# Kernel optimization log

Hardware: AMD Instinct MI355X
Metric: run time of the kernel (lower is better)

Reference implementation:

```python
import jax, jax.numpy as jnp
import numpy as np

B, C, H, W = 64, 128, 11, 11
OUT = 16
N_SIM = 5
EPS = 1e-2


def _conv3d(x, w, b):
    # x: [b,ci,D,h,w], w: [co,ci,7,3,3], 'same' padding, ReLU
    y = jax.lax.conv_general_dilated(x, w, (1, 1, 1), [(3, 3), (1, 1), (1, 1)],
                                     dimension_numbers=('NCDHW', 'OIDHW', 'NCDHW'))
    return jax.nn.relu(y + b[None, :, None, None, None])


def _conv2d(x, w, b, dil=1):
    p = dil  # 3x3 kernel, 'same' with dilation
    y = jax.lax.conv_general_dilated(x, w, (1, 1), [(p, p), (p, p)], rhs_dilation=(dil, dil),
                                     dimension_numbers=('NCHW', 'OIHW', 'NCHW'))
    return y + b[None, :, None, None]


def _center(f):  # [b,c,h,w] -> [b,c] (center pixel)
    return f[:, :, f.shape[2] // 2, f.shape[3] // 2]


def _ratio(v):  # compute_ratio_withstep: [b,c] -> [b,1,c,c] band-ratio image
    d = v[:, None, :]
    d = jnp.where(jnp.abs(d) < EPS, EPS, d)
    return (v[:, :, None] / d)[:, None, :, :]


def _cpr(sa3d, w):  # CVT3D_2D_SA: spectral-attention collapse [b,16,D,h,w] -> [b,16,h,w]
    a = jax.nn.softmax(w, axis=-1)
    return jax.nn.relu(jnp.einsum('bodhw,od->bohw', sa3d, a))


def _sideout(f2d, w, b):  # sideout2d: mlp on center pixel features
    return _center(f2d) @ w.T + b


def _similar_sum(x, feat, n=N_SIM):
    # topk(n, largest=False) over |feat - center|, gather those pixels from x, sum them
    b, c = x.shape[0], x.shape[1]
    cv = _center(feat).reshape(b, 1, 1, 1)
    diff = jnp.abs(feat - cv).reshape(b, -1)          # [b, h*w]
    _, idx = jax.lax.top_k(-diff, n)                   # n smallest -> [b, n]
    img = x.reshape(b, c, -1)                          # [b, c, h*w]
    idx_b = jnp.broadcast_to(idx[:, None, :], (b, c, n))
    sim = jnp.take_along_axis(img, idx_b, axis=2)      # [b, c, n]
    return sim.sum(axis=2)                             # masked sum over n similar pixels


def _forward(x, w3d1, b3d1, w3d23, b3d23, cpr_w, w2d45, b2d45, seg_w, seg_b,
             so_w, so_b, sp_wa, sp_ba, sp_wb, sp_bb, sp_sw, sp_sb, fuse_para):
    sp_ct = _ratio(_center(x))                         # [b,1,c,c]
    sa1 = _conv3d(x[:, None], w3d1, b3d1)              # [b,16,C,11,11]
    sa1_2d = _cpr(sa1, cpr_w[0])
    sa2 = _conv3d(sa1, w3d23[0], b3d23[0])
    sa2_2d = _cpr(sa2, cpr_w[1])
    sa3 = _conv3d(sa2, w3d23[1], b3d23[1])
    sa3_2d = _cpr(sa3, cpr_w[2])
    sa4_2d = jax.nn.relu(_conv2d(sa3_2d, w2d45[0], b2d45[0]))
    sa5_2d = jax.nn.relu(_conv2d(sa4_2d, w2d45[1], b2d45[1]))

    feats = [sa1_2d, sa2_2d, sa3_2d, sa4_2d, sa5_2d]
    sa_sides, sp_sides = [], []
    for i, f in enumerate(feats):  # fixed 5 structurally-distinct stages
        sa_sides.append(_sideout(f, so_w[i], so_b[i]))
        act = _conv2d(f, seg_w[i], seg_b[i])           # Seg_Conv: [b,1,11,11]
        s = _similar_sum(x, act)                       # [b,C]
        img = jnp.concatenate([_ratio(s), sp_ct], 1)   # [b,2,C,C]
        y = jax.nn.relu(_conv2d(img, sp_wa[i], sp_ba[i], dil=1))
        y = jax.nn.relu(_conv2d(y, sp_wb[i], sp_bb[i], dil=2))
        sp_sides.append(_sideout(y, sp_sw[i], sp_sb[i]))

    sides = sa_sides + sp_sides
    total = sides[0] * fuse_para[0]
    for i in range(1, 10):
        total = total + fuse_para[i] * sides[i]
    return total                                       # [b, OUT]


def setup_inputs() -> dict:
    key = jax.random.key(0)
    ks = jax.random.split(key, 20)
    s = 0.05
    return {
        'x': jax.random.normal(ks[0], (B, C, H, W), jnp.float32),
        'w3d1': jax.random.normal(ks[1], (16, 1, 7, 3, 3), jnp.float32) * s,
        'b3d1': jnp.zeros((16,), jnp.float32),
        'w3d23': jax.random.normal(ks[2], (2, 16, 16, 7, 3, 3), jnp.float32) * s,
        'b3d23': jnp.zeros((2, 16), jnp.float32),
        'cpr_w': jax.random.normal(ks[3], (3, 16, C), jnp.float32) * s,
        'w2d45': jax.random.normal(ks[4], (2, 16, 16, 3, 3), jnp.float32) * s,
        'b2d45': jnp.zeros((2, 16), jnp.float32),
        'seg_w': jax.random.normal(ks[5], (5, 1, 16, 3, 3), jnp.float32) * s,
        'seg_b': jnp.zeros((5, 1), jnp.float32),
        'so_w': jax.random.normal(ks[6], (5, OUT, 16), jnp.float32) * s,
        'so_b': jnp.zeros((5, OUT), jnp.float32),
        'sp_wa': jax.random.normal(ks[7], (5, 16, 2, 3, 3), jnp.float32) * s,
        'sp_ba': jnp.zeros((5, 16), jnp.float32),
        'sp_wb': jax.random.normal(ks[8], (5, 16, 16, 3, 3), jnp.float32) * s,
        'sp_bb': jnp.zeros((5, 16), jnp.float32),
        'sp_sw': jax.random.normal(ks[9], (5, OUT, 16), jnp.float32) * s,
        'sp_sb': jnp.zeros((5, OUT), jnp.float32),
        'fuse_para': jnp.ones((15,), jnp.float32),
    }


def reference(x, w3d1, b3d1, w3d23, b3d23, cpr_w, w2d45, b2d45, seg_w, seg_b,
              so_w, so_b, sp_wa, sp_ba, sp_wb, sp_bb, sp_sw, sp_sb, fuse_para):
    return _forward(x, w3d1, b3d1, w3d23, b3d23, cpr_w, w2d45, b2d45, seg_w, seg_b,
                    so_w, so_b, sp_wa, sp_ba, sp_wb, sp_bb, sp_sw, sp_sb, fuse_para)
```

## Files before the change

### kernel.cpp

```cpp
#include <hip/hip_runtime.h>
#include <hip/hip_bf16.h>


#define F_SLICE (64 * 16 * 121)
#define PKE (64 * 121 * 134 * 16)
#define LHALF 18304
#define AREP_CV 36864
#define XPADE (64 * 121 * 136)

typedef _Float16 half8 __attribute__((ext_vector_type(8)));
typedef float float4v __attribute__((ext_vector_type(4)));
typedef unsigned short u16x8 __attribute__((ext_vector_type(8)));
typedef unsigned short u16x4 __attribute__((ext_vector_type(4)));

typedef __attribute__((address_space(1))) unsigned int gu32;
typedef __attribute__((address_space(3))) unsigned int lu32;

union HU { _Float16 h; unsigned short u; };

__global__ __launch_bounds__(256) void prep_kernel(
    const float* __restrict__ x, const float* __restrict__ cpr_w,
    const float* __restrict__ w3d1, const float* __restrict__ w2d45,
    const float* __restrict__ w3d23, float* __restrict__ x_t,
    float* __restrict__ a_sm, float* __restrict__ wrep2d,
    unsigned short* __restrict__ arep, unsigned short* __restrict__ arep1,
    unsigned short* __restrict__ xpadh, unsigned short* __restrict__ xpadl,
    unsigned short* __restrict__ zpage) {
  const int bx = blockIdx.x, t = threadIdx.x;
  if (bx < 64) {
    __shared__ float tile[128][123];
    const int b = bx;
    const float* xb = x + (size_t)b * 128 * 121;
    for (int idx = t; idx < 128 * 121; idx += 256) {
      int c = idx / 121, p = idx - c * 121;
      tile[c][p] = xb[idx];
    }
    __syncthreads();
    float* ob = x_t + (size_t)b * 121 * 128;
    for (int idx = t; idx < 121 * 128; idx += 256) {
      int p = idx >> 7, c = idx & 127;
      ob[idx] = tile[c][p];
    }
    unsigned short* xh = xpadh + (size_t)b * 16456;
    unsigned short* xl = xpadl + (size_t)b * 16456;
    for (int idx = t; idx < 16456; idx += 256) {
      int p = idx / 136, d = idx - p * 136;
      float v = 0.f;
      if (d >= 3 && d < 131) v = tile[d - 3][p] * 256.f;
      _Float16 hi = (_Float16)v;
      HU a2, b2;
      a2.h = hi;
      b2.h = (_Float16)(v - (float)hi);
      xh[idx] = a2.u;
      xl[idx] = b2.u;
    }
  } else if (bx < 112) {
    __shared__ float red[128];
    const int row = bx - 64;
    float v = (t < 128) ? cpr_w[row * 128 + t] : -3.0e38f;
    if (t < 128) red[t] = v;
    __syncthreads();
    for (int s = 64; s; s >>= 1) {
      if (t < s) red[t] = fmaxf(red[t], red[t + s]);
      __syncthreads();
    }
    float m = red[0];
    __syncthreads();
    float e = (t < 128) ? expf(v - m) : 0.f;
    if (t < 128) red[t] = e;
    __syncthreads();
    for (int s = 64; s; s >>= 1) {
      if (t < s) red[t] += red[t + s];
      __syncthreads();
    }
    if (t < 128) a_sm[row * 128 + t] = e / red[0];
  } else if (bx < 142) {
    int r = (bx - 112) * 256 + t;
    if (r < 3072) {
      int j = r & 7;
      int lane = (r >> 3) & 63;
      int part = (r >> 9) & 1;
      int kh = r >> 10;
      int m = lane & 15, q = lane >> 4;
      float w = 0.f;
      if (q < 3 && j < 7) w = w3d1[m * 63 + j * 9 + kh * 3 + q] * 256.f;
      _Float16 hi = (_Float16)w;
      HU o;
      o.h = part ? (_Float16)(w - (float)hi) : hi;
      arep1[r] = o.u;
    } else if (r < 3072 + 4608) {
      int r2 = r - 3072;
      int o = r2 & 15;
      int uv = (r2 >> 4) % 9;
      int ic = (r2 / 144) % 16;
      int layer = r2 / 2304;
      wrep2d[r2] = w2d45[((layer * 16 + o) * 16 + ic) * 9 + uv];
    }
  } else if (bx < 430) {
    int idx = (bx - 142) * 256 + t;
    if (idx < 2 * AREP_CV) {
      int j = idx & 7;
      int lane = (idx >> 3) & 63;
      int part = (idx >> 9) & 1;
      int rem = idx >> 10;
      int chunk = rem % 36;
      int cv = rem / 36;
      int kw = chunk % 3;
      int grp = chunk / 3;
      int kdp = grp & 3;
      int kh = grp >> 2;
      int m = lane & 15, q = lane >> 4;
      int kd = 2 * kdp + (q >> 1);
      int ic = (q & 1) * 8 + j;
      float w = 0.f;
      if (kd < 7)
        w = w3d23[((cv * 16 + m) * 16 + ic) * 63 + kd * 9 + kh * 3 + kw] *
            256.f;
      _Float16 hi = (_Float16)w;
      HU out;
      out.h = (part == 0) ? hi : (_Float16)(w - (float)hi);
      arep[idx] = out.u;
    }
  } else {
    if (t < 128) {
      u16x8 z = {0, 0, 0, 0, 0, 0, 0, 0};
      *(u16x8*)&zpage[t * 8] = z;
    }
  }
}

__global__ __launch_bounds__(512, 2) void conv1_mfma_kernel(
    const unsigned short* __restrict__ xph,
    const unsigned short* __restrict__ xpl,
    const unsigned short* __restrict__ arep1, const float* __restrict__ bias,
    const float* __restrict__ al, unsigned short* __restrict__ pk_hi,
    unsigned short* __restrict__ pk_lo, float* __restrict__ fpart) {
  __shared__ _Float16 lds1[104 * 256];
  const int t = threadIdx.x;
  const int bx = blockIdx.x, gy = blockIdx.y, b = blockIdx.z;
  const int lane = t & 63, wave = t >> 6;
  const int n = lane & 15, q = lane >> 4;
  const int hs = wave >> 2, wg = wave & 3;
  const int h = 2 * bx + hs;
  const int D0 = gy * 32;

  {
    const int g = t & 31;
    const int s = g & 7;
    const int w0 = t >> 5;
#pragma unroll
    for (int k = 0; k < 7; ++k) {
      int wid = w0 + k * 16;
      if (wid < 104) {
        int part = wid >= 52;
        int w2 = wid - part * 52;
        int rr = w2 / 13;
        int cc = w2 - rr * 13;
        int hh = 2 * bx - 1 + rr, ww = cc - 1;
        u16x8 v0 = {0, 0, 0, 0, 0, 0, 0, 0};
        u16x8 v1 = {0, 0, 0, 0, 0, 0, 0, 0};
        if (hh >= 0 && hh < 11 && ww >= 0 && ww < 11) {
          const unsigned short* src = (part ? xpl : xph) +
                                      ((size_t)b * 121 + hh * 11 + ww) * 136 +
                                      D0 + (g & ~7);
          v0 = *(const u16x8*)src;
          v1 = *(const u16x8*)(src + 8);
        }
        u16x8 ov;
#define SHIFT_CASE(S)                                                   \
  case S: {                                                             \
    _Pragma("unroll") for (int e = 0; e < 8; ++e) ov[e] =               \
        (((S) + e) < 8) ? v0[((S) + e) & 7] : v1[((S) + e) & 7];        \
  } break;
        switch (s) {
          SHIFT_CASE(0)
          SHIFT_CASE(1)
          SHIFT_CASE(2)
          SHIFT_CASE(3)
          SHIFT_CASE(4)
          SHIFT_CASE(5)
          SHIFT_CASE(6)
          SHIFT_CASE(7)
        }
#undef SHIFT_CASE
        *(u16x8*)&lds1[wid * 256 + g * 8] = ov;
      }
    }
  }

  half8 ahi[3], alo[3];
#pragma unroll
  for (int kh = 0; kh < 3; ++kh) {
    ahi[kh] = *(const half8*)&arep1[(kh * 2 + 0) * 512 + lane * 8];
    alo[kh] = *(const half8*)&arep1[(kh * 2 + 1) * 512 + lane * 8];
  }
  int colq[3];
#pragma unroll
  for (int tt = 0; tt < 3; ++tt) {
    int c = wg * 3 + tt + q;
    colq[tt] = (c > 12) ? 12 : c;
  }
  float bias_r[4];
#pragma unroll
  for (int r = 0; r < 4; ++r) bias_r[r] = bias[q * 4 + r];
  __syncthreads();

#pragma unroll
  for (int d16loc = 0; d16loc < 2; ++d16loc) {
    const int d16g = gy * 2 + d16loc;
    const int dbase = d16loc * 16 + n;
    float4v acc[3];
#pragma unroll
    for (int tt = 0; tt < 3; ++tt) acc[tt] = (float4v){0.f, 0.f, 0.f, 0.f};
#pragma unroll
    for (int kh = 0; kh < 3; ++kh) {
      const int rowoff = (hs + kh) * 13;
#pragma unroll
      for (int tt = 0; tt < 3; ++tt) {
        const int wid = rowoff + colq[tt];
        half8 bh = *(const half8*)&lds1[wid * 256 + dbase * 8];
        half8 bl = *(const half8*)&lds1[(wid + 52) * 256 + dbase * 8];
        acc[tt] =
            __builtin_amdgcn_mfma_f32_16x16x32_f16(ahi[kh], bh, acc[tt], 0, 0, 0);
        acc[tt] =
            __builtin_amdgcn_mfma_f32_16x16x32_f16(ahi[kh], bl, acc[tt], 0, 0, 0);
        acc[tt] =
            __builtin_amdgcn_mfma_f32_16x16x32_f16(alo[kh], bh, acc[tt], 0, 0, 0);
      }
    }
    float alr[4];
#pragma unroll
    for (int r = 0; r < 4; ++r)
      alr[r] = al[(q * 4 + r) * 128 + d16g * 16 + n];
#pragma unroll
    for (int tt = 0; tt < 3; ++tt) {
      const int wl = wg * 3 + tt;
      if (h < 11 && wl < 11) {
        const int p = h * 11 + wl;
        float fr[4];
        u16x4 hi4, lo4;
#pragma unroll
        for (int r = 0; r < 4; ++r) {
          float sv = fmaxf(acc[tt][r] * (1.f / 65536.f) + bias_r[r], 0.f);
          fr[r] = sv * alr[r];
          float sc = sv * 256.f;
          _Float16 hh = (_Float16)sc;
          HU a2, b2;
          a2.h = hh;
          b2.h = (_Float16)(sc - (float)hh);
          hi4[r] = a2.u;
          lo4[r] = b2.u;
        }
        size_t base =
            (((size_t)b * 121 + p) * 134 + d16g * 16 + n + 3) * 16 + q * 4;
        *(u16x4*)&pk_hi[base] = hi4;
        *(u16x4*)&pk_lo[base] = lo4;
        u16x4 z = {0, 0, 0, 0};
        if (d16g == 0 && n < 3) {
          size_t hb = (((size_t)b * 121 + p) * 134 + n) * 16 + q * 4;
          *(u16x4*)&pk_hi[hb] = z;
          *(u16x4*)&pk_lo[hb] = z;
        }
        if (d16g == 7 && n >= 13) {
          size_t hb = (((size_t)b * 121 + p) * 134 + n + 118) * 16 + q * 4;
          *(u16x4*)&pk_hi[hb] = z;
          *(u16x4*)&pk_lo[hb] = z;
        }
#pragma unroll
        for (int r = 0; r < 4; ++r) {
          float v = fr[r];
          v += __shfl_xor(v, 1, 64);
          v += __shfl_xor(v, 2, 64);
          v += __shfl_xor(v, 4, 64);
          v += __shfl_xor(v, 8, 64);
          if (n == 0)
            fpart[(((size_t)d16g * 64 + b) * 16 + q * 4 + r) * 121 + p] = v;
        }
      }
    }
  }
}

template <bool WRITE_PK>
__global__ __launch_bounds__(512, 2) void conv_mfma_kernel(
    const unsigned short* __restrict__ pin_hi,
    const unsigned short* __restrict__ pin_lo,
    const unsigned short* __restrict__ arep, const float* __restrict__ bias,
    const float* __restrict__ al, const unsigned short* __restrict__ zpage,
    unsigned short* __restrict__ pout_hi, unsigned short* __restrict__ pout_lo,
    float* __restrict__ fpart) {
  __shared__ _Float16 lds[2 * LHALF];
  const int t = threadIdx.x;
  const int bx = blockIdx.x, d16 = blockIdx.y, b = blockIdx.z;
  const int lane = t & 63, wave = t >> 6;
  const int n = lane & 15, q = lane >> 4;
  const int hs = wave >> 2, wg = wave & 3;
  const int h = 2 * bx + hs;

#pragma unroll
  for (int i = 0; i < 9; ++i) {
    int u = t + i * 512;
    int lbo = __builtin_amdgcn_readfirstlane((wave << 6) + i * 512);
    if (u < 4576) {
      int part = (u >= 2288) ? 1 : 0;
      int qq = u - part * 2288;
      int panel = qq / 44;
      int rem = qq - panel * 44;
      int dloc = rem >> 1;
      int icq = rem & 1;
      int rr = panel / 13, cc = panel - rr * 13;
      int hh = 2 * bx + rr - 1, ww = cc - 1;
      bool ok = (hh >= 0) & (hh < 11) & (ww >= 0) & (ww < 11);
      const unsigned short* srcp = part ? pin_lo : pin_hi;
      const unsigned short* g =
          ok ? &srcp[(((size_t)b * 121 + hh * 11 + ww) * 134 + d16 * 16 +
                      dloc) *
                         16 +
                     icq * 8]
             : zpage;
      __builtin_amdgcn_global_load_lds((const gu32*)g,
                                       (lu32*)&lds[(size_t)lbo * 8], 16, 0, 0);
    }
  }
  float bias_r[4], alr[4];
#pragma unroll
  for (int r = 0; r < 4; ++r) {
    bias_r[r] = bias[q * 4 + r];
    alr[r] = al[(q * 4 + r) * 128 + d16 * 16 + n];
  }
  __syncthreads();

  const int wl0 = wg * 3;
  int cb[5], cbk[5];
  const int base_qn = (q & 1) * 8 + n * 16 + hs * 4576;
  const int kdh = (lane & 32) ? 16 : 0;
#pragma unroll
  for (int j = 0; j < 5; ++j) {
    int colj = wl0 + j;
    if (colj > 12) colj = 12;
    cb[j] = base_qn + colj * 352;
    cbk[j] = cb[j] + kdh;
  }

  float4v acc[3];
#pragma unroll
  for (int tt = 0; tt < 3; ++tt) acc[tt] = (float4v){0.f, 0.f, 0.f, 0.f};

#pragma unroll
  for (int kh = 0; kh < 3; ++kh) {
#pragma unroll
    for (int kdp = 0; kdp < 4; ++kdp) {
      half8 whi[5], wlo[5];
#pragma unroll
      for (int j = 0; j < 5; ++j) {
        int a = ((kdp < 3) ? cbk[j] : cb[j]) + kh * 4576 + kdp * 32;
        whi[j] = *(const half8*)&lds[a];
        wlo[j] = *(const half8*)&lds[a + LHALF];
      }
#pragma unroll
      for (int kw = 0; kw < 3; ++kw) {
        const int c2 = (kh * 4 + kdp) * 3 + kw;
        half8 ahi = *(const half8*)&arep[((c2 * 2 + 0) * 64 + lane) * 8];
        half8 alo = *(const half8*)&arep[((c2 * 2 + 1) * 64 + lane) * 8];
#pragma unroll
        for (int tt = 0; tt < 3; ++tt) {
          const int jj = tt + kw;
          acc[tt] = __builtin_amdgcn_mfma_f32_16x16x32_f16(ahi, whi[jj],
                                                           acc[tt], 0, 0, 0);
          acc[tt] = __builtin_amdgcn_mfma_f32_16x16x32_f16(ahi, wlo[jj],
                                                           acc[tt], 0, 0, 0);
          acc[tt] = __builtin_amdgcn_mfma_f32_16x16x32_f16(alo, whi[jj],
                                                           acc[tt], 0, 0, 0);
        }
      }
    }
  }

#pragma unroll
  for (int tt = 0; tt < 3; ++tt) {
    const int wl = wg * 3 + tt;
    if (h < 11 && wl < 11) {
      const int p = h * 11 + wl;
      float fr[4];
      u16x4 hi4, lo4;
#pragma unroll
      for (int r = 0; r < 4; ++r) {
        float sv = fmaxf(acc[tt][r] * (1.f / 65536.f) + bias_r[r], 0.f);
        fr[r] = sv * alr[r];
        if (WRITE_PK) {
          float s = sv * 256.f;
          _Float16 hh = (_Float16)s;
          HU a, bb;
          a.h = hh;
          bb.h = (_Float16)(s - (float)hh);
          hi4[r] = a.u;
          lo4[r] = bb.u;
        }
      }
      if (WRITE_PK) {
        size_t base =
            (((size_t)b * 121 + p) * 134 + d16 * 16 + n + 3) * 16 + q * 4;
        *(u16x4*)&pout_hi[base] = hi4;
        *(u16x4*)&pout_lo[base] = lo4;
        u16x4 z = {0, 0, 0, 0};
        if (d16 == 0 && n < 3) {
          size_t hb = (((size_t)b * 121 + p) * 134 + n) * 16 + q * 4;
          *(u16x4*)&pout_hi[hb] = z;
          *(u16x4*)&pout_lo[hb] = z;
        }
        if (d16 == 7 && n >= 13) {
          size_t hb = (((size_t)b * 121 + p) * 134 + n + 118) * 16 + q * 4;
          *(u16x4*)&pout_hi[hb] = z;
          *(u16x4*)&pout_lo[hb] = z;
        }
      }
#pragma unroll
      for (int r = 0; r < 4; ++r) {
        float v = fr[r];
        v += __shfl_xor(v, 1, 64);
        v += __shfl_xor(v, 2, 64);
        v += __shfl_xor(v, 4, 64);
        v += __shfl_xor(v, 8, 64);
        if (n == 0)
          fpart[(((size_t)d16 * 64 + b) * 16 + q * 4 + r) * 121 + p] = v;
      }
    }
  }
}

__global__ __launch_bounds__(128) void sp_prep_kernel(
    const float* __restrict__ fpart0, const float* __restrict__ fpart1,
    const float* __restrict__ fpart2, const float* __restrict__ x_t,
    const float* __restrict__ wrep2d, const float* __restrict__ b2d45,
    const float* __restrict__ seg_w, const float* __restrict__ seg_b,
    const float* __restrict__ so_w, const float* __restrict__ so_b,
    const float* __restrict__ sp_wa, const float* __restrict__ sp_ba,
    const float* __restrict__ sp_wb, const float* __restrict__ sp_bb,
    const float* __restrict__ sp_sw, const float* __restrict__ sp_sb,
    float* __restrict__ sa_sd, float* __restrict__ sp_sd) {
  const int b = blockIdx.x, i = blockIdx.y;
  const int t = threadIdx.x;
  __shared__ float fl[16 * 121];
  __shared__ float buf[16 * 121];
  __shared__ float act[121];
  __shared__ float diffs[121];
  __shared__ int sel[5];
  __shared__ float s7[7], xc7[7];
  __shared__ float P[2][7][7];
  __shared__ float y1[16][9];
  __shared__ float y2[16];

  {
    float* ldst = (i < 3) ? fl : buf;
    const float* fp0 = (i == 0) ? fpart0 : (i == 1) ? fpart1 : fpart2;
    const size_t boff = (size_t)b * 16 * 121;
    for (int idx = t; idx < 16 * 121; idx += 128) {
      float s = 0.f;
#pragma unroll
      for (int d16 = 0; d16 < 8; ++d16)
        s += fp0[(size_t)d16 * F_SLICE + boff + idx];
      ldst[idx] = fmaxf(s, 0.f);
    }
  }
  __syncthreads();

#define CONV2D_LAYER(SRC, DST, L)                                        \
  if (t < 121) {                                                         \
    int h_ = t / 11, w_ = t - h_ * 11;                                   \
    float a_[16];                                                        \
    _Pragma("unroll") for (int o = 0; o < 16; ++o) a_[o] =               \
        b2d45[(L)*16 + o];                                               \
    for (int ic = 0; ic < 16; ++ic) {                                    \
      _Pragma("unroll") for (int u = 0; u < 3; ++u) {                    \
        int hh_ = h_ + u - 1;                                            \
        _Pragma("unroll") for (int v = 0; v < 3; ++v) {                  \
          int ww_ = w_ + v - 1;                                          \
          float val_ = (hh_ >= 0 && hh_ < 11 && ww_ >= 0 && ww_ < 11)    \
                           ? (SRC)[ic * 121 + hh_ * 11 + ww_]            \
                           : 0.f;                                        \
          const float* wp_ =                                             \
              wrep2d + (((L)*16 + ic) * 9 + u * 3 + v) * 16;             \
          float wr_[16];                                                 \
          _Pragma("unroll") for (int o = 0; o < 16; ++o) wr_[o] = wp_[o];\
          _Pragma("unroll") for (int o = 0; o < 16; ++o) a_[o] =         \
              fmaf(val_, wr_[o], a_[o]);                                 \
        }                                                                \
      }                                                                  \
    }                                                                    \
    _Pragma("unroll") for (int o = 0; o < 16; ++o)(DST)[o * 121 + t] =   \
        fmaxf(a_[o], 0.f);                                               \
  }

  if (i >= 3) {
    CONV2D_LAYER(buf, fl, 0)
    __syncthreads();
    if (i == 4) {
      CONV2D_LAYER(fl, buf, 1)
      __syncthreads();
    }
  }
  const float* F = (i == 4) ? buf : fl;

  if (t < 16) {
    float s = so_b[i * 16 + t];
    const float* swp = so_w + (i * 16 + t) * 16;
    for (int c = 0; c < 16; ++c) s += F[c * 121 + 60] * swp[c];
    sa_sd[((size_t)i * 64 + b) * 16 + t] = s;
  }

  if (t < 121) {
    int h = t / 11, w = t - h * 11;
    float a = seg_b[i];
    const float* sw = seg_w + i * 144;
    for (int ic = 0; ic < 16; ++ic) {
      float w9[9];
#pragma unroll
      for (int j = 0; j < 9; ++j) w9[j] = sw[ic * 9 + j];
#pragma unroll
      for (int u = 0; u < 3; ++u) {
        int hh = h + u - 1;
#pragma unroll
        for (int v = 0; v < 3; ++v) {
          int ww = w + v - 1;
          if (hh >= 0 && hh < 11 && ww >= 0 && ww < 11)
            a = fmaf(F[ic * 121 + hh * 11 + ww], w9[u * 3 + v], a);
        }
      }
    }
    act[t] = a;
  }
  __syncthreads();
  if (t < 121) diffs[t] = fabsf(act[t] - act[60]);
  __syncthreads();

  for (int k = 0; k < 5; ++k) {
    if (t < 64) {
      float d0 = diffs[t];
      int i0 = t;
      float d1 = (t + 64 < 121) ? diffs[t + 64] : 3.0e38f;
      if (d1 < d0) { d0 = d1; i0 = t + 64; }
#pragma unroll
      for (int off = 32; off; off >>= 1) {
        float od = __shfl_down(d0, off, 64);
        int oi = __shfl_down(i0, off, 64);
        if (od < d0 || (od == d0 && oi < i0)) { d0 = od; i0 = oi; }
      }
      if (t == 0) {
        sel[k] = i0;
        diffs[i0] = 3.0e38f;
      }
    }
    __syncthreads();
  }

  if (t < 7) {
    const float* xb = x_t + (size_t)b * 121 * 128;
    float s = 0.f;
    for (int k = 0; k < 5; ++k) s += xb[(size_t)sel[k] * 128 + 61 + t];
    s7[t] = s;
    xc7[t] = xb[60 * 128 + 61 + t];
  }
  __syncthreads();
  if (t < 49) {
    int r = t / 7, c = t - r * 7;
    float d0 = s7[c];
    if (fabsf(d0) < 0.01f) d0 = 0.01f;
    float d1 = xc7[c];
    if (fabsf(d1) < 0.01f) d1 = 0.01f;
    P[0][r][c] = s7[r] / d0;
    P[1][r][c] = xc7[r] / d1;
  }
  __syncthreads();
  for (int item = t; item < 144; item += 128) {
    int ch = item / 9, pos = item - ch * 9;
    int a0 = pos / 3, b0 = pos - a0 * 3;
    float a = sp_ba[i * 16 + ch];
    const float* wa = sp_wa + ((size_t)(i * 16 + ch) * 2) * 9;
#pragma unroll
    for (int icc = 0; icc < 2; ++icc)
#pragma unroll
      for (int u = 0; u < 3; ++u)
#pragma unroll
        for (int v = 0; v < 3; ++v)
          a = fmaf(P[icc][2 * a0 + u][2 * b0 + v], wa[icc * 9 + u * 3 + v], a);
    y1[ch][pos] = fmaxf(a, 0.f);
  }
  __syncthreads();
  if (t < 16) {
    float a = sp_bb[i * 16 + t];
    const float* wb = sp_wb + (size_t)(i * 16 + t) * 16 * 9;
    for (int ch = 0; ch < 16; ++ch)
#pragma unroll
      for (int pos = 0; pos < 9; ++pos)
        a = fmaf(y1[ch][pos], wb[ch * 9 + pos], a);
    y2[t] = fmaxf(a, 0.f);
  }
  __syncthreads();
  if (t < 16) {
    float a = sp_sb[i * 16 + t];
    const float* swp = sp_sw + (size_t)(i * 16 + t) * 16;
    for (int ch = 0; ch < 16; ++ch) a = fmaf(y2[ch], swp[ch], a);
    sp_sd[((size_t)i * 64 + b) * 16 + t] = a;
  }
}

__global__ __launch_bounds__(256) void fuse_kernel(
    const float* __restrict__ sa_sd, const float* __restrict__ sp_sd,
    const float* __restrict__ fp, float* __restrict__ out) {
  int g = blockIdx.x * 256 + threadIdx.x;
  if (g >= 1024) return;
  int b = g >> 4, o = g & 15;
  float tot = 0.f;
  for (int i = 0; i < 5; ++i) {
    tot += fp[i] * sa_sd[((size_t)i * 64 + b) * 16 + o];
    tot += fp[5 + i] * sp_sd[((size_t)i * 64 + b) * 16 + o];
  }
  out[g] = tot;
}

extern "C" void kernel_launch(void* const* d_in, const int* in_sizes, int n_in,
                              void* d_out, int out_size, void* d_ws,
                              size_t ws_size, hipStream_t stream) {
  const float* x = (const float*)d_in[0];
  const float* w3d1 = (const float*)d_in[1];
  const float* b3d1 = (const float*)d_in[2];
  const float* w3d23 = (const float*)d_in[3];
  const float* b3d23 = (const float*)d_in[4];
  const float* cpr_w = (const float*)d_in[5];
  const float* w2d45 = (const float*)d_in[6];
  const float* b2d45 = (const float*)d_in[7];
  const float* seg_w = (const float*)d_in[8];
  const float* seg_b = (const float*)d_in[9];
  const float* so_w = (const float*)d_in[10];
  const float* so_b = (const float*)d_in[11];
  const float* sp_wa = (const float*)d_in[12];
  const float* sp_ba = (const float*)d_in[13];
  const float* sp_wb = (const float*)d_in[14];
  const float* sp_bb = (const float*)d_in[15];
  const float* sp_sw = (const float*)d_in[16];
  const float* sp_sb = (const float*)d_in[17];
  const float* fpar = (const float*)d_in[18];

  float* ws = (float*)d_ws;
  float* x_t = ws;
  float* a_sm = x_t + 991232;
  float* fpart0 = a_sm + 6144;
  float* fpart1 = fpart0 + 8 * F_SLICE;
  float* fpart2 = fpart1 + 8 * F_SLICE;
  float* sp_sd = fpart2 + 8 * F_SLICE;
  float* sa_sd = sp_sd + 5120;
  float* wrep2d = sa_sd + 5120;
  unsigned short* pk1h = (unsigned short*)(wrep2d + 4608);
  unsigned short* pk1l = pk1h + PKE;
  unsigned short* pk2h = pk1l + PKE;
  unsigned short* pk2l = pk2h + PKE;
  unsigned short* arep = pk2l + PKE;
  unsigned short* arep1 = arep + 2 * AREP_CV;
  unsigned short* zpage = arep1 + 3072;
  unsigned short* xpadh = (unsigned short*)fpart1;
  unsigned short* xpadl = xpadh + XPADE;

  prep_kernel<<<431, 256, 0, stream>>>(x, cpr_w, w3d1, w2d45, w3d23, x_t,
                                       a_sm, wrep2d, arep, arep1, xpadh,
                                       xpadl, zpage);

  conv1_mfma_kernel<<<dim3(6, 4, 64), 512, 0, stream>>>(
      xpadh, xpadl, arep1, b3d1, a_sm, pk1h, pk1l, fpart0);
  conv_mfma_kernel<true><<<dim3(6, 8, 64), 512, 0, stream>>>(
      pk1h, pk1l, arep, b3d23, a_sm + 2048, zpage, pk2h, pk2l, fpart1);
  conv_mfma_kernel<false><<<dim3(6, 8, 64), 512, 0, stream>>>(
      pk2h, pk2l, arep + AREP_CV, b3d23 + 16, a_sm + 4096, zpage, nullptr,
      nullptr, fpart2);

  sp_prep_kernel<<<dim3(64, 5), 128, 0, stream>>>(
      fpart0, fpart1, fpart2, x_t, wrep2d, b2d45, seg_w, seg_b, so_w, so_b,
      sp_wa, sp_ba, sp_wb, sp_bb, sp_sw, sp_sb, sa_sd, sp_sd);
  fuse_kernel<<<4, 256, 0, stream>>>(sa_sd, sp_sd, fpar, (float*)d_out);
}
```

Before: 420.7 us.

## Split conv LDS fill into hi/lo halves and overlap lo load with hi MFMAs

Each wave now loads a contiguous chunk of the LDS staging buffer, so waves 0-3 fill the hi half and waves 4-7 the lo half. Instead of one full barrier, the kernel waits only for the hi half, runs the hi-weight MFMA passes, then waits for the lo half and runs the hi-times-lo pass. The A operands from global memory are also prefetched one step ahead. This aims to hide part of the global-to-LDS load latency behind compute. It relies on inline vmcnt waits and raw s_barrier being correct, and the step-wise prefetch raises register pressure.

```diff
diff --git a/kernel.cpp b/kernel.cpp
--- a/kernel.cpp
+++ b/kernel.cpp
@@ -297,29 +297,32 @@
   const int hs = wave >> 2, wg = wave & 3;
   const int h = 2 * bx + hs;
 
-#pragma unroll
-  for (int i = 0; i < 9; ++i) {
-    int u = t + i * 512;
-    int lbo = __builtin_amdgcn_readfirstlane((wave << 6) + i * 512);
-    if (u < 4576) {
-      int part = (u >= 2288) ? 1 : 0;
-      int qq = u - part * 2288;
-      int panel = qq / 44;
-      int rem = qq - panel * 44;
-      int dloc = rem >> 1;
-      int icq = rem & 1;
-      int rr = panel / 13, cc = panel - rr * 13;
-      int hh = 2 * bx + rr - 1, ww = cc - 1;
-      bool ok = (hh >= 0) & (hh < 11) & (ww >= 0) & (ww < 11);
-      const unsigned short* srcp = part ? pin_lo : pin_hi;
-      const unsigned short* g =
-          ok ? &srcp[(((size_t)b * 121 + hh * 11 + ww) * 134 + d16 * 16 +
-                      dloc) *
-                         16 +
-                     icq * 8]
-             : zpage;
-      __builtin_amdgcn_global_load_lds((const gu32*)g,
-                                       (lu32*)&lds[(size_t)lbo * 8], 16, 0, 0);
+  {
+    const int ub = wave * 572;
+#pragma unroll
+    for (int it = 0; it < 9; ++it) {
+      const int lbo = __builtin_amdgcn_readfirstlane(ub + it * 64);
+      const int u = lbo + lane;
+      if (it < 8 || lane < 60) {
+        int part = (u >= 2288) ? 1 : 0;
+        int qq = u - part * 2288;
+        int panel = qq / 44;
+        int rem = qq - panel * 44;
+        int dloc = rem >> 1;
+        int icq = rem & 1;
+        int rr = panel / 13, cc = panel - rr * 13;
+        int hh = 2 * bx + rr - 1, ww = cc - 1;
+        bool ok = (hh >= 0) & (hh < 11) & (ww >= 0) & (ww < 11);
+        const unsigned short* srcp = part ? pin_lo : pin_hi;
+        const unsigned short* g =
+            ok ? &srcp[(((size_t)b * 121 + hh * 11 + ww) * 134 + d16 * 16 +
+                        dloc) *
+                           16 +
+                       icq * 8]
+               : zpage;
+        __builtin_amdgcn_global_load_lds(
+            (const gu32*)g, (lu32*)&lds[(size_t)lbo * 8], 16, 0, 0);
+      }
     }
   }
   float bias_r[4], alr[4];
@@ -328,7 +331,6 @@
     bias_r[r] = bias[q * 4 + r];
     alr[r] = al[(q * 4 + r) * 128 + d16 * 16 + n];
   }
-  __syncthreads();
 
   const int wl0 = wg * 3;
   int cb[5], cbk[5];
@@ -342,39 +344,88 @@
     cbk[j] = cb[j] + kdh;
   }
 
+  if (wave < 4) asm volatile("s_waitcnt vmcnt(0)" ::: "memory");
+  __builtin_amdgcn_sched_barrier(0);
+  __builtin_amdgcn_s_barrier();
+  __builtin_amdgcn_sched_barrier(0);
+
   float4v acc[3];
 #pragma unroll
   for (int tt = 0; tt < 3; ++tt) acc[tt] = (float4v){0.f, 0.f, 0.f, 0.f};
 
-#pragma unroll
-  for (int kh = 0; kh < 3; ++kh) {
-#pragma unroll
-    for (int kdp = 0; kdp < 4; ++kdp) {
-      half8 whi[5], wlo[5];
+#define LD_AH(c2) (*(const half8*)&arep[(((c2) * 2 + 0) * 64 + lane) * 8])
+#define LD_AL(c2) (*(const half8*)&arep[(((c2) * 2 + 1) * 64 + lane) * 8])
+
+  {
+    half8 Ah0 = LD_AH(0), Ah1 = LD_AH(1), Ah2 = LD_AH(2);
+    half8 Al0 = LD_AL(0), Al1 = LD_AL(1), Al2 = LD_AL(2);
+#pragma unroll
+    for (int s = 0; s < 12; ++s) {
+      const int kh = s >> 2, kdp = s & 3;
+      half8 bh[5];
 #pragma unroll
       for (int j = 0; j < 5; ++j) {
         int a = ((kdp < 3) ? cbk[j] : cb[j]) + kh * 4576 + kdp * 32;
-        whi[j] = *(const half8*)&lds[a];
-        wlo[j] = *(const half8*)&lds[a + LHALF];
-      }
-#pragma unroll
-      for (int kw = 0; kw < 3; ++kw) {
-        const int c2 = (kh * 4 + kdp) * 3 + kw;
-        half8 ahi = *(const half8*)&arep[((c2 * 2 + 0) * 64 + lane) * 8];
-        half8 alo = *(const half8*)&arep[((c2 * 2 + 1) * 64 + lane) * 8];
-#pragma unroll
-        for (int tt = 0; tt < 3; ++tt) {
-          const int jj = tt + kw;
-          acc[tt] = __builtin_amdgcn_mfma_f32_16x16x32_f16(ahi, whi[jj],
-                                                           acc[tt], 0, 0, 0);
-          acc[tt] = __builtin_amdgcn_mfma_f32_16x16x32_f16(ahi, wlo[jj],
-                                                           acc[tt], 0, 0, 0);
-          acc[tt] = __builtin_amdgcn_mfma_f32_16x16x32_f16(alo, whi[jj],
-                                                           acc[tt], 0, 0, 0);
-        }
-      }
-    }
-  }
+        bh[j] = *(const half8*)&lds[a];
+      }
+      const int sn = (s < 11) ? s + 1 : 11;
+      half8 nAh0 = LD_AH(sn * 3 + 0), nAh1 = LD_AH(sn * 3 + 1),
+            nAh2 = LD_AH(sn * 3 + 2);
+      half8 nAl0 = LD_AL(sn * 3 + 0), nAl1 = LD_AL(sn * 3 + 1),
+            nAl2 = LD_AL(sn * 3 + 2);
+#pragma unroll
+      for (int tt = 0; tt < 3; ++tt) {
+        acc[tt] =
+            __builtin_amdgcn_mfma_f32_16x16x32_f16(Ah0, bh[tt], acc[tt], 0, 0, 0);
+        acc[tt] =
+            __builtin_amdgcn_mfma_f32_16x16x32_f16(Al0, bh[tt], acc[tt], 0, 0, 0);
+        acc[tt] = __builtin_amdgcn_mfma_f32_16x16x32_f16(Ah1, bh[tt + 1],
+                                                         acc[tt], 0, 0, 0);
+        acc[tt] = __builtin_amdgcn_mfma_f32_16x16x32_f16(Al1, bh[tt + 1],
+                                                         acc[tt], 0, 0, 0);
+        acc[tt] = __builtin_amdgcn_mfma_f32_16x16x32_f16(Ah2, bh[tt + 2],
+                                                         acc[tt], 0, 0, 0);
+        acc[tt] = __builtin_amdgcn_mfma_f32_16x16x32_f16(Al2, bh[tt + 2],
+                                                         acc[tt], 0, 0, 0);
+      }
+      Ah0 = nAh0; Ah1 = nAh1; Ah2 = nAh2;
+      Al0 = nAl0; Al1 = nAl1; Al2 = nAl2;
+    }
+  }
+
+  if (wave >= 4) asm volatile("s_waitcnt vmcnt(0)" ::: "memory");
+  __builtin_amdgcn_sched_barrier(0);
+  __builtin_amdgcn_s_barrier();
+  __builtin_amdgcn_sched_barrier(0);
+
+  {
+    half8 Ah0 = LD_AH(0), Ah1 = LD_AH(1), Ah2 = LD_AH(2);
+#pragma unroll
+    for (int s = 0; s < 12; ++s) {
+      const int kh = s >> 2, kdp = s & 3;
+      half8 bl[5];
+#pragma unroll
+      for (int j = 0; j < 5; ++j) {
+        int a = ((kdp < 3) ? cbk[j] : cb[j]) + kh * 4576 + kdp * 32;
+        bl[j] = *(const half8*)&lds[a + LHALF];
+      }
+      const int sn = (s < 11) ? s + 1 : 11;
+      half8 nAh0 = LD_AH(sn * 3 + 0), nAh1 = LD_AH(sn * 3 + 1),
+            nAh2 = LD_AH(sn * 3 + 2);
+#pragma unroll
+      for (int tt = 0; tt < 3; ++tt) {
+        acc[tt] =
+            __builtin_amdgcn_mfma_f32_16x16x32_f16(Ah0, bl[tt], acc[tt], 0, 0, 0);
+        acc[tt] = __builtin_amdgcn_mfma_f32_16x16x32_f16(Ah1, bl[tt + 1],
+                                                         acc[tt], 0, 0, 0);
+        acc[tt] = __builtin_amdgcn_mfma_f32_16x16x32_f16(Ah2, bl[tt + 2],
+                                                         acc[tt], 0, 0, 0);
+      }
+      Ah0 = nAh0; Ah1 = nAh1; Ah2 = nAh2;
+    }
+  }
+#undef LD_AH
+#undef LD_AL
 
 #pragma unroll
   for (int tt = 0; tt < 3; ++tt) {
```

New measurement: 491.7 us. 16.9% more time.

## Halve conv LDS footprint by staging hi and lo input halves sequentially

Applied to the files above, without the earlier changes.

The conv MFMA kernel now stages only the hi half of the split-fp16 input into LDS, runs the hi-weight MFMA passes, then reloads the same buffer with the lo half and runs the remaining pass. This halves shared memory per block and raises the launch-bounds occupancy hint from 2 to 8, so more blocks can be resident per CU. The cost is two extra barriers, a serialized second global-to-LDS load with no overlap, repeated LDS fragment reads, and tighter register limits that may cause spills.

```diff
diff --git a/kernel.cpp b/kernel.cpp
--- a/kernel.cpp
+++ b/kernel.cpp
@@ -282,14 +282,14 @@
 }
 
 template <bool WRITE_PK>
-__global__ __launch_bounds__(512, 2) void conv_mfma_kernel(
+__global__ __launch_bounds__(512, 8) void conv_mfma_kernel(
     const unsigned short* __restrict__ pin_hi,
     const unsigned short* __restrict__ pin_lo,
     const unsigned short* __restrict__ arep, const float* __restrict__ bias,
     const float* __restrict__ al, const unsigned short* __restrict__ zpage,
     unsigned short* __restrict__ pout_hi, unsigned short* __restrict__ pout_lo,
     float* __restrict__ fpart) {
-  __shared__ _Float16 lds[2 * LHALF];
+  __shared__ _Float16 lds[LHALF];
   const int t = threadIdx.x;
   const int bx = blockIdx.x, d16 = blockIdx.y, b = blockIdx.z;
   const int lane = t & 63, wave = t >> 6;
@@ -297,38 +297,37 @@
   const int hs = wave >> 2, wg = wave & 3;
   const int h = 2 * bx + hs;
 
-#pragma unroll
-  for (int i = 0; i < 9; ++i) {
-    int u = t + i * 512;
-    int lbo = __builtin_amdgcn_readfirstlane((wave << 6) + i * 512);
-    if (u < 4576) {
-      int part = (u >= 2288) ? 1 : 0;
-      int qq = u - part * 2288;
-      int panel = qq / 44;
-      int rem = qq - panel * 44;
-      int dloc = rem >> 1;
-      int icq = rem & 1;
-      int rr = panel / 13, cc = panel - rr * 13;
-      int hh = 2 * bx + rr - 1, ww = cc - 1;
-      bool ok = (hh >= 0) & (hh < 11) & (ww >= 0) & (ww < 11);
-      const unsigned short* srcp = part ? pin_lo : pin_hi;
-      const unsigned short* g =
-          ok ? &srcp[(((size_t)b * 121 + hh * 11 + ww) * 134 + d16 * 16 +
-                      dloc) *
-                         16 +
-                     icq * 8]
-             : zpage;
-      __builtin_amdgcn_global_load_lds((const gu32*)g,
-                                       (lu32*)&lds[(size_t)lbo * 8], 16, 0, 0);
-    }
-  }
+#define STAGE_PART(SRCP)                                                      \
+  {                                                                           \
+    _Pragma("unroll") for (int it = 0; it < 5; ++it) {                        \
+      const int lbo = __builtin_amdgcn_readfirstlane((wave << 6) + it * 512); \
+      const int v = lbo + lane;                                               \
+      if (it < 4 || v < 2288) {                                               \
+        int panel = v / 44;                 \
+        int rem = v - panel * 44;                            \
+        int dloc = rem >> 1;                                                  \
+        int icq = rem & 1;                                                    \
+        int rr = panel / 13, cc = panel - rr * 13;                            \
+        int hh = 2 * bx + rr - 1, ww = cc - 1;                                \
+        bool ok = (hh >= 0) & (hh < 11) & (ww >= 0) & (ww < 11);              \
+        const unsigned short* g =                                             \
+            ok ? &(SRCP)[(((size_t)b * 121 + hh * 11 + ww) * 134 +            \
+                          d16 * 16 + dloc) * 16 + icq * 8]                    \
+               : zpage;                                                       \
+        __builtin_amdgcn_global_load_lds(                                     \
+            (const gu32*)g, (lu32*)&lds[(size_t)lbo * 8], 16, 0, 0);          \
+      }                                                                       \
+    }                                                                         \
+  }
+
+  STAGE_PART(pin_hi);
+
   float bias_r[4], alr[4];
 #pragma unroll
   for (int r = 0; r < 4; ++r) {
     bias_r[r] = bias[q * 4 + r];
     alr[r] = al[(q * 4 + r) * 128 + d16 * 16 + n];
   }
-  __syncthreads();
 
   const int wl0 = wg * 3;
   int cb[5], cbk[5];
@@ -346,16 +345,17 @@
 #pragma unroll
   for (int tt = 0; tt < 3; ++tt) acc[tt] = (float4v){0.f, 0.f, 0.f, 0.f};
 
+  __syncthreads();
+
 #pragma unroll
   for (int kh = 0; kh < 3; ++kh) {
 #pragma unroll
     for (int kdp = 0; kdp < 4; ++kdp) {
-      half8 whi[5], wlo[5];
+      half8 bf[5];
 #pragma unroll
       for (int j = 0; j < 5; ++j) {
         int a = ((kdp < 3) ? cbk[j] : cb[j]) + kh * 4576 + kdp * 32;
-        whi[j] = *(const half8*)&lds[a];
-        wlo[j] = *(const half8*)&lds[a + LHALF];
+        bf[j] = *(const half8*)&lds[a];
       }
 #pragma unroll
       for (int kw = 0; kw < 3; ++kw) {
@@ -365,16 +365,43 @@
 #pragma unroll
         for (int tt = 0; tt < 3; ++tt) {
           const int jj = tt + kw;
-          acc[tt] = __builtin_amdgcn_mfma_f32_16x16x32_f16(ahi, whi[jj],
+          acc[tt] = __builtin_amdgcn_mfma_f32_16x16x32_f16(ahi, bf[jj],
                                                            acc[tt], 0, 0, 0);
-          acc[tt] = __builtin_amdgcn_mfma_f32_16x16x32_f16(ahi, wlo[jj],
+          acc[tt] = __builtin_amdgcn_mfma_f32_16x16x32_f16(alo, bf[jj],
                                                            acc[tt], 0, 0, 0);
-          acc[tt] = __builtin_amdgcn_mfma_f32_16x16x32_f16(alo, whi[jj],
+        }
+      }
+    }
+  }
+
+  __syncthreads();
+  STAGE_PART(pin_lo);
+  __syncthreads();
+
+#pragma unroll
+  for (int kh = 0; kh < 3; ++kh) {
+#pragma unroll
+    for (int kdp = 0; kdp < 4; ++kdp) {
+      half8 bf[5];
+#pragma unroll
+      for (int j = 0; j < 5; ++j) {
+        int a = ((kdp < 3) ? cbk[j] : cb[j]) + kh * 4576 + kdp * 32;
+        bf[j] = *(const half8*)&lds[a];
+      }
+#pragma unroll
+      for (int kw = 0; kw < 3; ++kw) {
+        const int c2 = (kh * 4 + kdp) * 3 + kw;
+        half8 ahi = *(const half8*)&arep[((c2 * 2 + 0) * 64 + lane) * 8];
+#pragma unroll
+        for (int tt = 0; tt < 3; ++tt) {
+          const int jj = tt + kw;
+          acc[tt] = __builtin_amdgcn_mfma_f32_16x16x32_f16(ahi, bf[jj],
                                                            acc[tt], 0, 0, 0);
         }
       }
     }
   }
+#undef STAGE_PART
 
 #pragma unroll
   for (int tt = 0; tt < 3; ++tt) {
```

Measured after the change: 581.2 us. +38.2%, slower.
